# Performance work log

Measured on AMD Instinct MI355X. Metric: run time of the kernel, lower is better.

## Reference

```python
import jax, jax.numpy as jnp
import numpy as np

N_NODES = 100000
N_EDGES = 1600000
N_GRAPHS = 256
F_IN = 38
HID = 64


def graph_conv(x, edge_index, w_rel, b_rel, w_root):
    # PyG GraphConv (aggr='add'): out = lin_rel(sum_{j in N(i)} x_j) + lin_root(x_i)
    src, dst = edge_index[0], edge_index[1]
    agg = jax.ops.segment_sum(x[src], dst, num_segments=N_NODES)  # [N, F]
    return agg @ w_rel + b_rel + x @ w_root


def setup_inputs() -> dict:
    key = jax.random.key(0)
    ks = jax.random.split(key, 10)
    x = jax.random.normal(ks[0], (N_NODES, F_IN), dtype=jnp.float32)
    edge_index = jax.random.randint(ks[1], (2, N_EDGES), 0, N_NODES, dtype=jnp.int64)
    batch = jnp.sort(jax.random.randint(ks[2], (N_NODES,), 0, N_GRAPHS, dtype=jnp.int64))
    s1 = 1.0 / np.sqrt(F_IN)
    s2 = 1.0 / np.sqrt(HID)
    w1_rel = jax.random.uniform(ks[3], (F_IN, HID), jnp.float32, -s1, s1)
    b1_rel = jax.random.uniform(ks[4], (HID,), jnp.float32, -s1, s1)
    w1_root = jax.random.uniform(ks[5], (F_IN, HID), jnp.float32, -s1, s1)
    w2_rel = jax.random.uniform(ks[6], (HID, HID), jnp.float32, -s2, s2)
    b2_rel = jax.random.uniform(ks[7], (HID,), jnp.float32, -s2, s2)
    w2_root = jax.random.uniform(ks[8], (HID, HID), jnp.float32, -s2, s2)
    return {"x": x, "edge_index": edge_index, "batch": batch,
            "w1_rel": w1_rel, "b1_rel": b1_rel, "w1_root": w1_root,
            "w2_rel": w2_rel, "b2_rel": b2_rel, "w2_root": w2_root}


def reference(x, edge_index, batch, w1_rel, b1_rel, w1_root, w2_rel, b2_rel, w2_root):
    h = graph_conv(x, edge_index, w1_rel, b1_rel, w1_root)
    h = jax.nn.relu(h)
    h = graph_conv(h, edge_index, w2_rel, b2_rel, w2_root)
    # global_mean_pool: segment mean over batch ids
    sums = jax.ops.segment_sum(h, batch, num_segments=N_GRAPHS)  # [G, HID]
    counts = jax.ops.segment_sum(jnp.ones((N_NODES,), h.dtype), batch, num_segments=N_GRAPHS)
    pooled = sums / jnp.maximum(counts, 1.0)[:, None]
    # dropout(p=0.5, training=False) is identity in eval mode
    return jax.nn.relu(pooled)
```

## Files before the change

### kernel.cpp

```cpp
#include <hip/hip_runtime.h>

#define N_NODES 100000
#define N_EDGES 1600000
#define N_GRAPHS 256
#define F_IN 38
#define F_PAD 40
#define HID 64
#define CAPD 48

#define NB   391
#define EPB  4096
#define EDGE_BLOCKS 391
#define PACK_BLOCKS 15626
#define BCAP 4608

typedef unsigned short ushort;
typedef unsigned int uint;
typedef _Float16 h2 __attribute__((ext_vector_type(2)));

__device__ __forceinline__ h2 u2h(uint u) {
    union { uint u; h2 h; } v; v.u = u; return v.h;
}
__device__ __forceinline__ uint h2u(h2 h) {
    union { uint u; h2 h; } v; v.h = h; return v.u;
}
__device__ __forceinline__ ushort f2h_bits(float f) {
    union { _Float16 h; ushort s; } v; v.h = (_Float16)f; return v.s;
}
__device__ __forceinline__ int clampi(int v) {
    return (int)min((uint)v, (uint)N_NODES);
}

__global__ __launch_bounds__(256, 4) void pre_kernel(
        const float* __restrict__ x,
        const int* __restrict__ src,
        const int* __restrict__ dst,
        int* __restrict__ gcur,
        uint* __restrict__ ebuf,
        ushort* __restrict__ xb,
        ushort* __restrict__ hb) {
    __shared__ int    hist[NB];
    __shared__ int    offs[NB];
    __shared__ int    cur[NB];
    __shared__ int    gbase[NB];
    __shared__ int    scan[512];
    __shared__ uint   sbuf[EPB];
    __shared__ ushort sb[EPB];

    const int blk = blockIdx.x;
    if (blk >= EDGE_BLOCKS) {
        int tid = (blk - EDGE_BLOCKS) * 256 + threadIdx.x;
        if (tid < HID) hb[(N_NODES << 6) + tid] = 0;
        if (tid >= (N_NODES + 1) * F_PAD) return;
        int n = tid / F_PAD;
        int f = tid - n * F_PAD;
        float v = (n < N_NODES && f < F_IN) ? x[n * F_IN + f] : 0.0f;
        xb[tid] = f2h_bits(v);
        return;
    }

    for (int i = threadIdx.x; i < NB; i += 256) hist[i] = 0;
    __syncthreads();

    const int base = blk * EPB + threadIdx.x;
    int  bkt[EPB / 256];
    uint pl[EPB / 256];
    #pragma unroll
    for (int i = 0; i < EPB / 256; ++i) {
        int e = base + i * 256;
        bkt[i] = -1;
        if (e < N_EDGES) {
            int d = dst[e];
            bkt[i] = d >> 8;
            pl[i] = ((uint)src[e] << 8) | ((uint)d & 255u);
            atomicAdd(&hist[bkt[i]], 1);
        }
    }
    __syncthreads();

    {
        int i0 = threadIdx.x, i1 = threadIdx.x + 256;
        scan[i0] = (i0 < NB) ? hist[i0] : 0;
        scan[i1] = (i1 < NB) ? hist[i1] : 0;
        __syncthreads();
        for (int d = 1; d < 512; d <<= 1) {
            int v0 = (i0 >= d) ? scan[i0 - d] : 0;
            int v1 = (i1 >= d) ? scan[i1 - d] : 0;
            __syncthreads();
            scan[i0] += v0;
            scan[i1] += v1;
            __syncthreads();
        }
    }
    for (int i = threadIdx.x; i < NB; i += 256) {
        int h = hist[i];
        int o = scan[i] - h;
        offs[i] = o;
        cur[i] = o;
        gbase[i] = (h > 0) ? atomicAdd(&gcur[i], h) : 0;
    }
    __syncthreads();

    #pragma unroll
    for (int i = 0; i < EPB / 256; ++i) {
        if (bkt[i] >= 0) {
            int pos = atomicAdd(&cur[bkt[i]], 1);
            sbuf[pos] = pl[i];
            sb[pos] = (ushort)bkt[i];
        }
    }
    __syncthreads();

    int total = scan[NB - 1];
    for (int i = threadIdx.x; i < total; i += 256) {
        int b = sb[i];
        int p = gbase[b] + (i - offs[b]);
        if (p < BCAP) ebuf[b * BCAP + p] = sbuf[i];
    }
}

__global__ __launch_bounds__(256, 3) void build_kernel(
        const uint* __restrict__ ebuf,
        const int* __restrict__ gcur,
        int* __restrict__ cnt,
        int* __restrict__ slots) {
    __shared__ int cl[256];
    __shared__ int s_slots[256 * CAPD];
    const int b = blockIdx.x;
    cl[threadIdx.x] = 0;
    for (int i = threadIdx.x; i < 256 * CAPD; i += 256) s_slots[i] = N_NODES;
    __syncthreads();
    int e1 = gcur[b]; if (e1 > BCAP) e1 = BCAP;
    for (int idx = threadIdx.x; idx < e1; idx += 256) {
        uint e = ebuf[b * BCAP + idx];
        int dl = (int)(e & 255u);
        int pos = atomicAdd(&cl[dl], 1);
        if (pos < CAPD) s_slots[dl * CAPD + pos] = (int)(e >> 8);
    }
    __syncthreads();
    int n = (b << 8) + threadIdx.x;
    if (n < N_NODES) cnt[n] = cl[threadIdx.x];
    int nrows = N_NODES - (b << 8);
    if (nrows > 256) nrows = 256;
    int lim = nrows * (CAPD / 4);
    const int4* sp = (const int4*)s_slots;
    int4* gp = (int4*)(slots + b * 256 * CAPD);
    for (int i = threadIdx.x; i < lim; i += 256) gp[i] = sp[i];
}

__global__ __launch_bounds__(256, 4) void layer1_kernel(
        const uint* __restrict__ xb32,
        const int* __restrict__ cnt,
        const int* __restrict__ slots,
        const float* __restrict__ w_rel,
        const float* __restrict__ b_rel,
        const float* __restrict__ w_root,
        const int* __restrict__ batch,
        ushort* __restrict__ hb,
        float* __restrict__ hsum) {
    __shared__ uint s_wrelp[20 * HID];
    __shared__ uint s_wrootp[20 * HID];
    __shared__ uint s_a[64][20];
    __shared__ uint s_x[64][20];
    for (int i = threadIdx.x; i < 20 * HID; i += 256) {
        int kk = i >> 6, cc = i & 63;
        int k0 = 2 * kk, k1 = 2 * kk + 1;
        float r0 = (k0 < F_IN) ? w_rel[k0 * HID + cc] : 0.f;
        float r1 = (k1 < F_IN) ? w_rel[k1 * HID + cc] : 0.f;
        float o0 = (k0 < F_IN) ? w_root[k0 * HID + cc] : 0.f;
        float o1 = (k1 < F_IN) ? w_root[k1 * HID + cc] : 0.f;
        s_wrelp[i]  = (uint)f2h_bits(r0) | ((uint)f2h_bits(r1) << 16);
        s_wrootp[i] = (uint)f2h_bits(o0) | ((uint)f2h_bits(o1) << 16);
    }
    const int wave = threadIdx.x >> 6, lane = threadIdx.x & 63;
    const int half = lane >> 5, l32 = lane & 31;
    const int base = blockIdx.x * 64;

    for (int i = 0; i < 8; ++i) {
        int nl = wave * 16 + 2 * i + half;
        int n = base + nl;
        uint xv = 0;
        int dp = 0;
        if (n < N_NODES) {
            int deg = cnt[n]; if (deg > CAPD) deg = CAPD;
            dp = (deg + 15) & ~15; if (dp > CAPD) dp = CAPD;
            if (l32 < 20) xv = xb32[n * 20 + l32];
        }
        h2 sum = {(_Float16)0, (_Float16)0};
        const int* sl = slots + n * CAPD;
        for (int j = 0; j < dp; j += 16) {
            int4 a4 = *(const int4*)(sl + j);
            int4 b4 = *(const int4*)(sl + j + 4);
            int4 c4 = *(const int4*)(sl + j + 8);
            int4 d4 = *(const int4*)(sl + j + 12);
            if (l32 < 20) {
                uint v0 = xb32[clampi(a4.x) * 20 + l32];
                uint v1 = xb32[clampi(a4.y) * 20 + l32];
                uint v2 = xb32[clampi(a4.z) * 20 + l32];
                uint v3 = xb32[clampi(a4.w) * 20 + l32];
                uint v4 = xb32[clampi(b4.x) * 20 + l32];
                uint v5 = xb32[clampi(b4.y) * 20 + l32];
                uint v6 = xb32[clampi(b4.z) * 20 + l32];
                uint v7 = xb32[clampi(b4.w) * 20 + l32];
                uint v8 = xb32[clampi(c4.x) * 20 + l32];
                uint v9 = xb32[clampi(c4.y) * 20 + l32];
                uint va = xb32[clampi(c4.z) * 20 + l32];
                uint vb = xb32[clampi(c4.w) * 20 + l32];
                uint vc = xb32[clampi(d4.x) * 20 + l32];
                uint vd = xb32[clampi(d4.y) * 20 + l32];
                uint ve = xb32[clampi(d4.z) * 20 + l32];
                uint vf = xb32[clampi(d4.w) * 20 + l32];
                h2 t0 = (u2h(v0) + u2h(v1)) + (u2h(v2) + u2h(v3));
                h2 t1 = (u2h(v4) + u2h(v5)) + (u2h(v6) + u2h(v7));
                h2 t2 = (u2h(v8) + u2h(v9)) + (u2h(va) + u2h(vb));
                h2 t3 = (u2h(vc) + u2h(vd)) + (u2h(ve) + u2h(vf));
                sum += (t0 + t1) + (t2 + t3);
            }
        }
        if (l32 < 20) {
            s_a[nl][l32] = h2u(sum);
            s_x[nl][l32] = xv;
        }
    }
    __syncthreads();

    const int c = lane, r = wave;
    const float bias = b_rel[c];
    float psum = 0.f;
    int cur_g = -1;
    for (int i = 0; i < 16; ++i) {
        int nl = r * 16 + i;
        int n = base + nl;
        if (n >= N_NODES) break;
        h2 acc = {(_Float16)0, (_Float16)0};
        #pragma unroll
        for (int k8 = 0; k8 < 5; ++k8) {
            uint4 pa = *(const uint4*)&s_a[nl][k8 * 4];
            uint4 px = *(const uint4*)&s_x[nl][k8 * 4];
            acc += u2h(pa.x) * u2h(s_wrelp[(k8 * 4 + 0) * HID + c]);
            acc += u2h(pa.y) * u2h(s_wrelp[(k8 * 4 + 1) * HID + c]);
            acc += u2h(pa.z) * u2h(s_wrelp[(k8 * 4 + 2) * HID + c]);
            acc += u2h(pa.w) * u2h(s_wrelp[(k8 * 4 + 3) * HID + c]);
            acc += u2h(px.x) * u2h(s_wrootp[(k8 * 4 + 0) * HID + c]);
            acc += u2h(px.y) * u2h(s_wrootp[(k8 * 4 + 1) * HID + c]);
            acc += u2h(px.z) * u2h(s_wrootp[(k8 * 4 + 2) * HID + c]);
            acc += u2h(px.w) * u2h(s_wrootp[(k8 * 4 + 3) * HID + c]);
        }
        float hv = fmaxf((float)acc.x + (float)acc.y + bias, 0.f);
        hb[(n << 6) + c] = f2h_bits(hv);
        int g = batch[n];
        if (g != cur_g) {
            if (cur_g >= 0) atomicAdd(&hsum[(cur_g << 6) + c], psum);
            psum = 0.f;
            cur_g = g;
        }
        psum += hv;
    }
    if (cur_g >= 0) atomicAdd(&hsum[(cur_g << 6) + c], psum);
}

__global__ __launch_bounds__(256, 8) void layer2_kernel(
        const uint* __restrict__ hb32,
        const int* __restrict__ cnt,
        const int* __restrict__ slots,
        const int* __restrict__ batch,
        float* __restrict__ esum) {
    const int wave = threadIdx.x >> 6, lane = threadIdx.x & 63;
    const int half = lane >> 5, l32 = lane & 31;
    const int base = blockIdx.x * 64;

    float psum0 = 0.f, psum1 = 0.f;
    int cur_g = -1;
    for (int i = 0; i < 8; ++i) {
        int n = base + wave * 16 + 2 * i + half;
        if (n < N_NODES) {
            int deg = cnt[n]; if (deg > CAPD) deg = CAPD;
            int dp = (deg + 15) & ~15; if (dp > CAPD) dp = CAPD;
            h2 sum = {(_Float16)0, (_Float16)0};
            const int* sl = slots + n * CAPD;
            for (int j = 0; j < dp; j += 16) {
                int4 a4 = *(const int4*)(sl + j);
                int4 b4 = *(const int4*)(sl + j + 4);
                int4 c4 = *(const int4*)(sl + j + 8);
                int4 d4 = *(const int4*)(sl + j + 12);
                uint v0 = hb32[(clampi(a4.x) << 5) + l32];
                uint v1 = hb32[(clampi(a4.y) << 5) + l32];
                uint v2 = hb32[(clampi(a4.z) << 5) + l32];
                uint v3 = hb32[(clampi(a4.w) << 5) + l32];
                uint v4 = hb32[(clampi(b4.x) << 5) + l32];
                uint v5 = hb32[(clampi(b4.y) << 5) + l32];
                uint v6 = hb32[(clampi(b4.z) << 5) + l32];
                uint v7 = hb32[(clampi(b4.w) << 5) + l32];
                uint v8 = hb32[(clampi(c4.x) << 5) + l32];
                uint v9 = hb32[(clampi(c4.y) << 5) + l32];
                uint va = hb32[(clampi(c4.z) << 5) + l32];
                uint vb = hb32[(clampi(c4.w) << 5) + l32];
                uint vc = hb32[(clampi(d4.x) << 5) + l32];
                uint vd = hb32[(clampi(d4.y) << 5) + l32];
                uint ve = hb32[(clampi(d4.z) << 5) + l32];
                uint vf = hb32[(clampi(d4.w) << 5) + l32];
                h2 t0 = (u2h(v0) + u2h(v1)) + (u2h(v2) + u2h(v3));
                h2 t1 = (u2h(v4) + u2h(v5)) + (u2h(v6) + u2h(v7));
                h2 t2 = (u2h(v8) + u2h(v9)) + (u2h(va) + u2h(vb));
                h2 t3 = (u2h(vc) + u2h(vd)) + (u2h(ve) + u2h(vf));
                sum += (t0 + t1) + (t2 + t3);
            }
            int g = batch[n];
            if (g != cur_g) {
                if (cur_g >= 0) {
                    atomicAdd(&esum[(cur_g << 6) + 2 * l32], psum0);
                    atomicAdd(&esum[(cur_g << 6) + 2 * l32 + 1], psum1);
                }
                psum0 = 0.f; psum1 = 0.f;
                cur_g = g;
            }
            psum0 += (float)sum.x;
            psum1 += (float)sum.y;
        }
    }
    if (cur_g >= 0) {
        atomicAdd(&esum[(cur_g << 6) + 2 * l32], psum0);
        atomicAdd(&esum[(cur_g << 6) + 2 * l32 + 1], psum1);
    }
}

__global__ void finalize_kernel(const float* __restrict__ esum,
                                const float* __restrict__ hsum,
                                const float* __restrict__ w2_rel,
                                const float* __restrict__ w2_root,
                                const float* __restrict__ b2,
                                const int* __restrict__ batch,
                                float* __restrict__ out) {
    __shared__ float s_e[HID];
    __shared__ float s_h[HID];
    const int g = blockIdx.x;
    const int c = threadIdx.x;
    s_e[c] = esum[(g << 6) + c];
    s_h[c] = hsum[(g << 6) + c];
    __syncthreads();

    int lo = 0, hi = N_NODES;
    while (lo < hi) { int m = (lo + hi) >> 1; if (batch[m] < g) lo = m + 1; else hi = m; }
    int start = lo;
    hi = N_NODES;
    while (lo < hi) { int m = (lo + hi) >> 1; if (batch[m] < g + 1) lo = m + 1; else hi = m; }
    int cntg = lo - start;

    float acc = (float)cntg * b2[c];
    #pragma unroll
    for (int k = 0; k < HID; ++k) {
        acc += s_e[k] * w2_rel[k * HID + c];
        acc += s_h[k] * w2_root[k * HID + c];
    }
    float denom = cntg > 0 ? (float)cntg : 1.f;
    out[(g << 6) + c] = fmaxf(acc / denom, 0.f);
}

extern "C" void kernel_launch(void* const* d_in, const int* in_sizes, int n_in,
                              void* d_out, int out_size, void* d_ws, size_t ws_size,
                              hipStream_t stream) {
    const float* x       = (const float*)d_in[0];
    const int*   ei      = (const int*)  d_in[1];
    const int*   batch   = (const int*)  d_in[2];
    const float* w1_rel  = (const float*)d_in[3];
    const float* b1_rel  = (const float*)d_in[4];
    const float* w1_root = (const float*)d_in[5];
    const float* w2_rel  = (const float*)d_in[6];
    const float* b2_rel  = (const float*)d_in[7];
    const float* w2_root = (const float*)d_in[8];
    float* out = (float*)d_out;

    const int* src = ei;
    const int* dst = ei + N_EDGES;

    char* wsb = (char*)d_ws;
    int*    cnt   = (int*)   (wsb);
    float*  hsum  = (float*) (wsb + 400000);
    float*  esum  = (float*) (wsb + 465536);
    int*    gcur  = (int*)   (wsb + 531072);
    int*    slots = (int*)   (wsb + 532640);
    ushort* xb    = (ushort*)(wsb + 19732640);
    ushort* hb    = (ushort*)(wsb + 27732720);
    uint*   ebuf  = (uint*)  (wsb + 27732720);

    hipMemsetAsync(wsb + 400000, 0, 132636, stream);

    {
        pre_kernel<<<EDGE_BLOCKS + PACK_BLOCKS, 256, 0, stream>>>(
            x, src, dst, gcur, ebuf, xb, hb);
    }
    build_kernel<<<NB, 256, 0, stream>>>(ebuf, gcur, cnt, slots);

    {
        int blocks = (N_NODES + 63) / 64;
        layer1_kernel<<<blocks, 256, 0, stream>>>((const uint*)xb, cnt, slots,
                                                  w1_rel, b1_rel, w1_root, batch,
                                                  hb, hsum);
    }
    {
        int blocks = (N_NODES + 63) / 64;
        layer2_kernel<<<blocks, 256, 0, stream>>>((const uint*)hb, cnt, slots,
                                                  batch, esum);
    }
    {
        finalize_kernel<<<N_GRAPHS, HID, 0, stream>>>(esum, hsum, w2_rel, w2_root,
                                                      b2_rel, batch, out);
    }
}
```

Before: 243.0 us.

## Fuse CSR slot building into layer kernels using shared-memory bucket scatter

Drops the separate build_kernel and its global slots/cnt arrays. Each layer kernel now rebuilds its neighbor lists for a 128-node half-bucket in shared memory from the bucketed edge buffer, then gathers features using those local slots. Blocks grow to 512 threads covering 128 nodes. This removes one launch and a global write/read of the slot table. In exchange, each bucket's edges are scanned twice per layer (once by each half-block) and twice overall, and shared memory use per block rises.

```diff
diff --git a/kernel.cpp b/kernel.cpp
--- a/kernel.cpp
+++ b/kernel.cpp
@@ -13,6 +13,7 @@
 #define EDGE_BLOCKS 391
 #define PACK_BLOCKS 15626
 #define BCAP 4608
+#define NBL  (2 * NB)
 
 typedef unsigned short ushort;
 typedef unsigned int uint;
@@ -119,39 +120,10 @@
     }
 }
 
-__global__ __launch_bounds__(256, 3) void build_kernel(
+__global__ __launch_bounds__(512, 8) void layer1_kernel(
+        const uint* __restrict__ xb32,
         const uint* __restrict__ ebuf,
         const int* __restrict__ gcur,
-        int* __restrict__ cnt,
-        int* __restrict__ slots) {
-    __shared__ int cl[256];
-    __shared__ int s_slots[256 * CAPD];
-    const int b = blockIdx.x;
-    cl[threadIdx.x] = 0;
-    for (int i = threadIdx.x; i < 256 * CAPD; i += 256) s_slots[i] = N_NODES;
-    __syncthreads();
-    int e1 = gcur[b]; if (e1 > BCAP) e1 = BCAP;
-    for (int idx = threadIdx.x; idx < e1; idx += 256) {
-        uint e = ebuf[b * BCAP + idx];
-        int dl = (int)(e & 255u);
-        int pos = atomicAdd(&cl[dl], 1);
-        if (pos < CAPD) s_slots[dl * CAPD + pos] = (int)(e >> 8);
-    }
-    __syncthreads();
-    int n = (b << 8) + threadIdx.x;
-    if (n < N_NODES) cnt[n] = cl[threadIdx.x];
-    int nrows = N_NODES - (b << 8);
-    if (nrows > 256) nrows = 256;
-    int lim = nrows * (CAPD / 4);
-    const int4* sp = (const int4*)s_slots;
-    int4* gp = (int4*)(slots + b * 256 * CAPD);
-    for (int i = threadIdx.x; i < lim; i += 256) gp[i] = sp[i];
-}
-
-__global__ __launch_bounds__(256, 4) void layer1_kernel(
-        const uint* __restrict__ xb32,
-        const int* __restrict__ cnt,
-        const int* __restrict__ slots,
         const float* __restrict__ w_rel,
         const float* __restrict__ b_rel,
         const float* __restrict__ w_root,
@@ -160,9 +132,10 @@
         float* __restrict__ hsum) {
     __shared__ uint s_wrelp[20 * HID];
     __shared__ uint s_wrootp[20 * HID];
-    __shared__ uint s_a[64][20];
-    __shared__ uint s_x[64][20];
-    for (int i = threadIdx.x; i < 20 * HID; i += 256) {
+    __shared__ int  s_slots[128 * CAPD];
+    __shared__ int  cl[128];
+
+    for (int i = threadIdx.x; i < 20 * HID; i += 512) {
         int kk = i >> 6, cc = i & 63;
         int k0 = 2 * kk, k1 = 2 * kk + 1;
         float r0 = (k0 < F_IN) ? w_rel[k0 * HID + cc] : 0.f;
@@ -172,22 +145,45 @@
         s_wrelp[i]  = (uint)f2h_bits(r0) | ((uint)f2h_bits(r1) << 16);
         s_wrootp[i] = (uint)f2h_bits(o0) | ((uint)f2h_bits(o1) << 16);
     }
+    const int b   = blockIdx.x >> 1;
+    const int dlo = (blockIdx.x & 1) << 7;
+    if (threadIdx.x < 128) cl[threadIdx.x] = 0;
+    {
+        int4* sp = (int4*)s_slots;
+        int4 dummy = make_int4(N_NODES, N_NODES, N_NODES, N_NODES);
+        for (int i = threadIdx.x; i < 128 * CAPD / 4; i += 512) sp[i] = dummy;
+    }
+    __syncthreads();
+    int e1 = gcur[b]; if (e1 > BCAP) e1 = BCAP;
+    for (int idx = threadIdx.x; idx < e1; idx += 512) {
+        uint e = ebuf[b * BCAP + idx];
+        int dl = (int)(e & 255u) - dlo;
+        if ((uint)dl < 128u) {
+            int pos = atomicAdd(&cl[dl], 1);
+            if (pos < CAPD) s_slots[dl * CAPD + pos] = (int)(e >> 8);
+        }
+    }
+    __syncthreads();
+
     const int wave = threadIdx.x >> 6, lane = threadIdx.x & 63;
     const int half = lane >> 5, l32 = lane & 31;
-    const int base = blockIdx.x * 64;
-
+    const int nbase = (b << 8) + dlo;
+
+    h2   sums[8];
+    uint xvs[8];
+    #pragma unroll
     for (int i = 0; i < 8; ++i) {
         int nl = wave * 16 + 2 * i + half;
-        int n = base + nl;
+        int n = nbase + nl;
         uint xv = 0;
         int dp = 0;
         if (n < N_NODES) {
-            int deg = cnt[n]; if (deg > CAPD) deg = CAPD;
+            int deg = cl[nl]; if (deg > CAPD) deg = CAPD;
             dp = (deg + 15) & ~15; if (dp > CAPD) dp = CAPD;
             if (l32 < 20) xv = xb32[n * 20 + l32];
         }
         h2 sum = {(_Float16)0, (_Float16)0};
-        const int* sl = slots + n * CAPD;
+        const int* sl = s_slots + nl * CAPD;
         for (int j = 0; j < dp; j += 16) {
             int4 a4 = *(const int4*)(sl + j);
             int4 b4 = *(const int4*)(sl + j + 4);
@@ -217,9 +213,18 @@
                 sum += (t0 + t1) + (t2 + t3);
             }
         }
+        sums[i] = sum;
+        xvs[i] = xv;
+    }
+    __syncthreads();
+    uint* s_a = (uint*)s_slots;
+    uint* s_x = ((uint*)s_slots) + 128 * 20;
+    #pragma unroll
+    for (int i = 0; i < 8; ++i) {
+        int nl = wave * 16 + 2 * i + half;
         if (l32 < 20) {
-            s_a[nl][l32] = h2u(sum);
-            s_x[nl][l32] = xv;
+            s_a[nl * 20 + l32] = h2u(sums[i]);
+            s_x[nl * 20 + l32] = xvs[i];
         }
     }
     __syncthreads();
@@ -230,13 +235,13 @@
     int cur_g = -1;
     for (int i = 0; i < 16; ++i) {
         int nl = r * 16 + i;
-        int n = base + nl;
+        int n = nbase + nl;
         if (n >= N_NODES) break;
         h2 acc = {(_Float16)0, (_Float16)0};
         #pragma unroll
         for (int k8 = 0; k8 < 5; ++k8) {
-            uint4 pa = *(const uint4*)&s_a[nl][k8 * 4];
-            uint4 px = *(const uint4*)&s_x[nl][k8 * 4];
+            uint4 pa = *(const uint4*)&s_a[nl * 20 + k8 * 4];
+            uint4 px = *(const uint4*)&s_x[nl * 20 + k8 * 4];
             acc += u2h(pa.x) * u2h(s_wrelp[(k8 * 4 + 0) * HID + c]);
             acc += u2h(pa.y) * u2h(s_wrelp[(k8 * 4 + 1) * HID + c]);
             acc += u2h(pa.z) * u2h(s_wrelp[(k8 * 4 + 2) * HID + c]);
@@ -259,25 +264,49 @@
     if (cur_g >= 0) atomicAdd(&hsum[(cur_g << 6) + c], psum);
 }
 
-__global__ __launch_bounds__(256, 8) void layer2_kernel(
+__global__ __launch_bounds__(512, 8) void layer2_kernel(
         const uint* __restrict__ hb32,
-        const int* __restrict__ cnt,
-        const int* __restrict__ slots,
+        const uint* __restrict__ ebuf,
+        const int* __restrict__ gcur,
         const int* __restrict__ batch,
         float* __restrict__ esum) {
+    __shared__ int s_slots[128 * CAPD];
+    __shared__ int cl[128];
+
+    const int b   = blockIdx.x >> 1;
+    const int dlo = (blockIdx.x & 1) << 7;
+    if (threadIdx.x < 128) cl[threadIdx.x] = 0;
+    {
+        int4* sp = (int4*)s_slots;
+        int4 dummy = make_int4(N_NODES, N_NODES, N_NODES, N_NODES);
+        for (int i = threadIdx.x; i < 128 * CAPD / 4; i += 512) sp[i] = dummy;
+    }
+    __syncthreads();
+    int e1 = gcur[b]; if (e1 > BCAP) e1 = BCAP;
+    for (int idx = threadIdx.x; idx < e1; idx += 512) {
+        uint e = ebuf[b * BCAP + idx];
+        int dl = (int)(e & 255u) - dlo;
+        if ((uint)dl < 128u) {
+            int pos = atomicAdd(&cl[dl], 1);
+            if (pos < CAPD) s_slots[dl * CAPD + pos] = (int)(e >> 8);
+        }
+    }
+    __syncthreads();
+
     const int wave = threadIdx.x >> 6, lane = threadIdx.x & 63;
     const int half = lane >> 5, l32 = lane & 31;
-    const int base = blockIdx.x * 64;
+    const int nbase = (b << 8) + dlo;
 
     float psum0 = 0.f, psum1 = 0.f;
     int cur_g = -1;
     for (int i = 0; i < 8; ++i) {
-        int n = base + wave * 16 + 2 * i + half;
+        int nl = wave * 16 + 2 * i + half;
+        int n = nbase + nl;
         if (n < N_NODES) {
-            int deg = cnt[n]; if (deg > CAPD) deg = CAPD;
+            int deg = cl[nl]; if (deg > CAPD) deg = CAPD;
             int dp = (deg + 15) & ~15; if (dp > CAPD) dp = CAPD;
             h2 sum = {(_Float16)0, (_Float16)0};
-            const int* sl = slots + n * CAPD;
+            const int* sl = s_slots + nl * CAPD;
             for (int j = 0; j < dp; j += 16) {
                 int4 a4 = *(const int4*)(sl + j);
                 int4 b4 = *(const int4*)(sl + j + 4);
@@ -374,33 +403,27 @@
     const int* dst = ei + N_EDGES;
 
     char* wsb = (char*)d_ws;
-    int*    cnt   = (int*)   (wsb);
-    float*  hsum  = (float*) (wsb + 400000);
-    float*  esum  = (float*) (wsb + 465536);
-    int*    gcur  = (int*)   (wsb + 531072);
-    int*    slots = (int*)   (wsb + 532640);
+    float*  hsum  = (float*) (wsb);
+    float*  esum  = (float*) (wsb + 65536);
+    int*    gcur  = (int*)   (wsb + 131072);
+    uint*   ebuf  = (uint*)  (wsb + 132672);
     ushort* xb    = (ushort*)(wsb + 19732640);
     ushort* hb    = (ushort*)(wsb + 27732720);
-    uint*   ebuf  = (uint*)  (wsb + 27732720);
-
-    hipMemsetAsync(wsb + 400000, 0, 132636, stream);
+
+    hipMemsetAsync(wsb, 0, 132636, stream);
 
     {
         pre_kernel<<<EDGE_BLOCKS + PACK_BLOCKS, 256, 0, stream>>>(
             x, src, dst, gcur, ebuf, xb, hb);
     }
-    build_kernel<<<NB, 256, 0, stream>>>(ebuf, gcur, cnt, slots);
-
-    {
-        int blocks = (N_NODES + 63) / 64;
-        layer1_kernel<<<blocks, 256, 0, stream>>>((const uint*)xb, cnt, slots,
-                                                  w1_rel, b1_rel, w1_root, batch,
-                                                  hb, hsum);
-    }
-    {
-        int blocks = (N_NODES + 63) / 64;
-        layer2_kernel<<<blocks, 256, 0, stream>>>((const uint*)hb, cnt, slots,
-                                                  batch, esum);
+    {
+        layer1_kernel<<<NBL, 512, 0, stream>>>((const uint*)xb, ebuf, gcur,
+                                               w1_rel, b1_rel, w1_root, batch,
+                                               hb, hsum);
+    }
+    {
+        layer2_kernel<<<NBL, 512, 0, stream>>>((const uint*)hb, ebuf, gcur,
+                                               batch, esum);
     }
     {
         finalize_kernel<<<N_GRAPHS, HID, 0, stream>>>(esum, hsum, w2_rel, w2_root,
```

Measured after the change: 228.8 us. 5.8% less time.
